# Kernel optimization log

Measured on AMD Instinct MI355X. Metric: run time of the kernel, lower is better.

The kernel has to match this reference:

```python
import jax, jax.numpy as jnp
import numpy as np
from jax import lax

B, T, H = 2, 1024, 2048
NH, D = 8, 128          # heads, head_dim
P = NH * D              # projection size
K = 4                   # short conv kernel size
EPS = 1e-6
SCALE = D ** -0.5


def _causal_conv_silu(x, w):
    # x: (B,T,C); w: (C,K) depthwise causal conv followed by silu (ShortConvolution)
    C = w.shape[0]
    kern = jnp.transpose(w)[:, None, :]  # (K,1,C)
    y = lax.conv_general_dilated(x, kern, window_strides=(1,), padding=[(K - 1, 0)],
                                 dimension_numbers=('NWC', 'WIO', 'NWC'),
                                 feature_group_count=C)
    return jax.nn.silu(y)


def _l2norm(x):
    return x * jax.lax.rsqrt(jnp.sum(x * x, axis=-1, keepdims=True) + EPS)


def _forward(hidden_states, Wq, Wk, Wv, conv_q, conv_k, conv_v, A_log, dt_bias,
             Wfa, Wfb, Wb, Wga, Wgb, norm_weight, Wo):
    x = hidden_states                                # (B,T,H)
    q = _causal_conv_silu(x @ Wq.T, conv_q)          # (B,T,P)
    k = _causal_conv_silu(x @ Wk.T, conv_k)
    v = _causal_conv_silu(x @ Wv.T, conv_v)
    # fused_kda_gate: g = -exp(A_log) * softplus(f_b(f_a(x)) + dt_bias), per (h,d) channel
    gf = (x @ Wfa.T) @ Wfb.T                         # (B,T,P) low-rank gate proj
    gf = gf.reshape(B, T, NH, D) + dt_bias.reshape(NH, D)
    g = -jnp.exp(A_log)[None, None, :, None] * jax.nn.softplus(gf)  # (B,T,NH,D) log-decay <= 0
    beta = jax.nn.sigmoid(x @ Wb.T)                  # (B,T,NH)
    q = _l2norm(q.reshape(B, T, NH, D)) * SCALE      # use_qk_l2norm_in_kernel + 1/sqrt(d) scale
    k = _l2norm(k.reshape(B, T, NH, D))
    v = v.reshape(B, T, NH, D)

    # gated delta-rule recurrence (KDA): per-key-channel decay, beta-weighted delta update
    def step(S, inp):
        q_t, k_t, v_t, g_t, b_t = inp                # (B,NH,D), beta (B,NH)
        S = S * jnp.exp(g_t)[..., None]              # decay rows (key dim) of S[.,.,dk,dv]
        kv = jnp.einsum('bhk,bhkv->bhv', k_t, S)
        delta = (v_t - kv) * b_t[..., None]
        S = S + jnp.einsum('bhk,bhv->bhkv', k_t, delta)
        o_t = jnp.einsum('bhk,bhkv->bhv', q_t, S)
        return S, o_t

    tfirst = lambda a: jnp.moveaxis(a, 1, 0)         # time-major for scan
    S0 = jnp.zeros((B, NH, D, D), x.dtype)
    _, o = lax.scan(step, S0, (tfirst(q), tfirst(k), tfirst(v), tfirst(g), tfirst(beta)))
    o = jnp.moveaxis(o, 0, 1)                        # (B,T,NH,D)

    # FusedRMSNormGated(sigmoid): gate applied before RMS normalization (Mamba2 convention)
    gate = ((x @ Wga.T) @ Wgb.T).reshape(B, T, NH, D)
    og = o * jax.nn.sigmoid(gate)
    og = og * jax.lax.rsqrt(jnp.mean(og * og, axis=-1, keepdims=True) + EPS) * norm_weight
    return og.reshape(B * T, P) @ Wo.T               # (B*T, H)


def setup_inputs():
    ks = jax.random.split(jax.random.key(0), 16)
    s = 0.02
    f32 = jnp.float32
    return {
        'hidden_states': jax.random.normal(ks[0], (B, T, H), f32),
        'Wq': jax.random.normal(ks[1], (P, H), f32) * s,
        'Wk': jax.random.normal(ks[2], (P, H), f32) * s,
        'Wv': jax.random.normal(ks[3], (P, H), f32) * s,
        'conv_q': jax.random.normal(ks[4], (P, K), f32) * 0.3,
        'conv_k': jax.random.normal(ks[5], (P, K), f32) * 0.3,
        'conv_v': jax.random.normal(ks[6], (P, K), f32) * 0.3,
        'A_log': jnp.log(jax.random.uniform(ks[7], (NH,), f32, 1.0, 16.0)),
        'dt_bias': jax.random.normal(ks[8], (P,), f32) * 0.5,
        'Wfa': jax.random.normal(ks[9], (D, H), f32) * s,
        'Wfb': jax.random.normal(ks[10], (P, D), f32) * s,
        'Wb': jax.random.normal(ks[11], (NH, H), f32) * s,
        'Wga': jax.random.normal(ks[12], (D, H), f32) * s,
        'Wgb': jax.random.normal(ks[13], (P, D), f32) * s,
        'norm_weight': jnp.ones((D,), f32),
        'Wo': jax.random.normal(ks[14], (H, P), f32) * s,
    }


def reference(hidden_states, Wq, Wk, Wv, conv_q, conv_k, conv_v, A_log, dt_bias,
              Wfa, Wfb, Wb, Wga, Wgb, norm_weight, Wo):
    return _forward(hidden_states, Wq, Wk, Wv, conv_q, conv_k, conv_v, A_log, dt_bias,
                    Wfa, Wfb, Wb, Wga, Wgb, norm_weight, Wo)
```

## Files before the change

### kernel.cpp

```cpp
#include <hip/hip_runtime.h>
#include <hip/hip_bf16.h>
#include <cstddef>
#include <cstdint>

#define Bb 2
#define Tt 1024
#define Hh 2048
#define NHh 8
#define Dd 128
#define Pp (NHh * Dd)
#define Kk 4
#define EPSf 1e-6f
#define SCALEf 0.08838834764831845f
#define DVQ 16
#define CHUNK 8

typedef short bf16x8 __attribute__((ext_vector_type(8)));
typedef float f32x4 __attribute__((ext_vector_type(4)));
typedef float f32x2 __attribute__((ext_vector_type(2)));

template <int CTRL>
__device__ __forceinline__ float dpp_add(float x) {
  int yi = __builtin_amdgcn_update_dpp(0, __builtin_bit_cast(int, x), CTRL, 0xF, 0xF, true);
  return x + __builtin_bit_cast(float, yi);
}
__device__ __forceinline__ float row16_sum(float x) {
  x = dpp_add<0xB1>(x);
  x = dpp_add<0x4E>(x);
  x = dpp_add<0x124>(x);
  x = dpp_add<0x128>(x);
  return x;
}

__device__ __forceinline__ void gload_lds16(const void* g, void* l) {
  __builtin_amdgcn_global_load_lds((const __attribute__((address_space(1))) void*)g,
                                   (__attribute__((address_space(3))) void*)l, 16, 0, 0);
}

__global__ __launch_bounds__(256) void cvt_bf16(const float* __restrict__ src,
                                                __hip_bfloat16* __restrict__ dst, int n) {
  const int i = (blockIdx.x * 256 + threadIdx.x) * 8;
  if (i >= n) return;
  const float4 a = *reinterpret_cast<const float4*>(src + i);
  const float4 b = *reinterpret_cast<const float4*>(src + i + 4);
  __hip_bfloat16 t[8];
  t[0] = __float2bfloat16(a.x); t[1] = __float2bfloat16(a.y);
  t[2] = __float2bfloat16(a.z); t[3] = __float2bfloat16(a.w);
  t[4] = __float2bfloat16(b.x); t[5] = __float2bfloat16(b.y);
  t[6] = __float2bfloat16(b.z); t[7] = __float2bfloat16(b.w);
  *reinterpret_cast<uint4*>(dst + i) = *reinterpret_cast<const uint4*>(t);
}

__global__ __launch_bounds__(256) void cvt_bf16_x4(const float* __restrict__ s0,
                                                   const float* __restrict__ s1,
                                                   const float* __restrict__ s2,
                                                   const float* __restrict__ s3,
                                                   __hip_bfloat16* __restrict__ d0,
                                                   __hip_bfloat16* __restrict__ d1,
                                                   __hip_bfloat16* __restrict__ d2,
                                                   __hip_bfloat16* __restrict__ d3,
                                                   int nper) {
  const int bpa = nper / 2048;
  const int a = blockIdx.x / bpa;
  const int i = (blockIdx.x % bpa) * 2048 + threadIdx.x * 8;
  const float* src = (a == 0) ? s0 : (a == 1) ? s1 : (a == 2) ? s2 : s3;
  __hip_bfloat16* dst = (a == 0) ? d0 : (a == 1) ? d1 : (a == 2) ? d2 : d3;
  const float4 x = *reinterpret_cast<const float4*>(src + i);
  const float4 y = *reinterpret_cast<const float4*>(src + i + 4);
  __hip_bfloat16 t[8];
  t[0] = __float2bfloat16(x.x); t[1] = __float2bfloat16(x.y);
  t[2] = __float2bfloat16(x.z); t[3] = __float2bfloat16(x.w);
  t[4] = __float2bfloat16(y.x); t[5] = __float2bfloat16(y.y);
  t[6] = __float2bfloat16(y.z); t[7] = __float2bfloat16(y.w);
  *reinterpret_cast<uint4*>(dst + i) = *reinterpret_cast<const uint4*>(t);
}

__global__ __launch_bounds__(256) void cvt_split(const float* __restrict__ src,
                                                 __hip_bfloat16* __restrict__ hi,
                                                 __hip_bfloat16* __restrict__ lo, int n) {
  const int i = (blockIdx.x * 256 + threadIdx.x) * 8;
  if (i >= n) return;
  __hip_bfloat16 th[8], tl[8];
#pragma unroll
  for (int j = 0; j < 2; j++) {
    const float4 a = *reinterpret_cast<const float4*>(src + i + j * 4);
    const float f[4] = {a.x, a.y, a.z, a.w};
#pragma unroll
    for (int e = 0; e < 4; e++) {
      const __hip_bfloat16 h = __float2bfloat16(f[e]);
      th[j * 4 + e] = h;
      tl[j * 4 + e] = __float2bfloat16(f[e] - __bfloat162float(h));
    }
  }
  *reinterpret_cast<uint4*>(hi + i) = *reinterpret_cast<const uint4*>(th);
  *reinterpret_cast<uint4*>(lo + i) = *reinterpret_cast<const uint4*>(tl);
}

__global__ __launch_bounds__(256) void transpose_f32(const float* __restrict__ src,
                                                     float* __restrict__ dst, int R, int C) {
  __shared__ float t[32][33];
  const int bx = blockIdx.x * 32, by = blockIdx.y * 32;
  const int tx = threadIdx.x & 31, ty = threadIdx.x >> 5;
#pragma unroll
  for (int i = ty; i < 32; i += 8) {
    const int r = by + i, c = bx + tx;
    if (r < R && c < C) t[i][tx] = src[(size_t)r * C + c];
  }
  __syncthreads();
#pragma unroll
  for (int i = ty; i < 32; i += 8) {
    const int c = bx + i, r = by + tx;
    if (c < C && r < R) dst[(size_t)c * R + r] = t[tx][i];
  }
}

__global__ __launch_bounds__(256) void gemm_bf16_lds(const __hip_bfloat16* __restrict__ A,
                                                     const __hip_bfloat16* __restrict__ B,
                                                     float* __restrict__ C,
                                                     __hip_bfloat16* __restrict__ Cbf,
                                                     int M, int N, int K, int outmode) {
  __shared__ __align__(16) __hip_bfloat16 As[128 * 64];
  __shared__ __align__(16) __hip_bfloat16 Bs[128 * 64];
  const int tid = threadIdx.x;
  const int wave = tid >> 6;
  const int lane = tid & 63;
  const int wm = (wave >> 1) * 64;
  const int wn = (wave & 1) * 64;
  const int bm = blockIdx.y * 128;
  const int bn = blockIdx.x * 128;
  const int l15 = lane & 15;
  const int l4 = lane >> 4;
  const int srow = lane >> 3;
  const int scol = (lane & 7) * 8;

  f32x4 acc[4][4];
#pragma unroll
  for (int i = 0; i < 4; i++)
#pragma unroll
    for (int j = 0; j < 4; j++) acc[i][j] = (f32x4){0.f, 0.f, 0.f, 0.f};

  for (int k0 = 0; k0 < K; k0 += 64) {
#pragma unroll
    for (int i = 0; i < 4; i++) {
      const int s = wave * 4 + i;
      const int row = s * 8 + srow;
      gload_lds16(A + (size_t)(bm + row) * K + k0 + scol, &As[s * 512]);
      gload_lds16(B + (size_t)(bn + row) * K + k0 + scol, &Bs[s * 512]);
    }
    __syncthreads();
    bf16x8 af[4][2], bfv[4][2];
#pragma unroll
    for (int kf = 0; kf < 2; kf++) {
      const int kc = kf * 32 + l4 * 8;
#pragma unroll
      for (int mf = 0; mf < 4; mf++)
        af[mf][kf] = *reinterpret_cast<const bf16x8*>(&As[(wm + mf * 16 + l15) * 64 + kc]);
#pragma unroll
      for (int nf = 0; nf < 4; nf++)
        bfv[nf][kf] = *reinterpret_cast<const bf16x8*>(&Bs[(wn + nf * 16 + l15) * 64 + kc]);
    }
#pragma unroll
    for (int kf = 0; kf < 2; kf++)
#pragma unroll
      for (int mf = 0; mf < 4; mf++)
#pragma unroll
        for (int nf = 0; nf < 4; nf++)
          acc[mf][nf] = __builtin_amdgcn_mfma_f32_16x16x32_bf16(af[mf][kf], bfv[nf][kf],
                                                                acc[mf][nf], 0, 0, 0);
    __syncthreads();
  }
#pragma unroll
  for (int mf = 0; mf < 4; mf++) {
#pragma unroll
    for (int nf = 0; nf < 4; nf++) {
      const int col = bn + wn + nf * 16 + l15;
#pragma unroll
      for (int r = 0; r < 4; r++) {
        const int row = bm + wm + mf * 16 + l4 * 4 + r;
        if (outmode == 0) C[(size_t)row * N + col] = acc[mf][nf][r];
        else Cbf[(size_t)row * N + col] = __float2bfloat16(acc[mf][nf][r]);
      }
    }
  }
}

__global__ __launch_bounds__(256) void gemm_bf16_3t_lds(const __hip_bfloat16* __restrict__ Ahi,
                                                        const __hip_bfloat16* __restrict__ Alo,
                                                        const __hip_bfloat16* __restrict__ Bhi,
                                                        const __hip_bfloat16* __restrict__ Blo,
                                                        float* __restrict__ C,
                                                        int M, int N, int K,
                                                        const float* __restrict__ dtb,
                                                        const float* __restrict__ A_log,
                                                        int gmode) {
  __shared__ __align__(16) __hip_bfloat16 Ahs[64 * 64];
  __shared__ __align__(16) __hip_bfloat16 Als[64 * 64];
  __shared__ __align__(16) __hip_bfloat16 Bhs[128 * 64];
  __shared__ __align__(16) __hip_bfloat16 Bls[128 * 64];
  const int tid = threadIdx.x;
  const int wave = tid >> 6;
  const int lane = tid & 63;
  const int wm = (wave >> 1) * 32;
  const int wn = (wave & 1) * 64;
  const int bm = blockIdx.y * 64;
  const int bn = blockIdx.x * 128;
  const int l15 = lane & 15;
  const int l4 = lane >> 4;
  const int srow = lane >> 3;
  const int scol = (lane & 7) * 8;

  f32x4 acc[2][4];
#pragma unroll
  for (int i = 0; i < 2; i++)
#pragma unroll
    for (int j = 0; j < 4; j++) acc[i][j] = (f32x4){0.f, 0.f, 0.f, 0.f};

  for (int k0 = 0; k0 < K; k0 += 64) {
#pragma unroll
    for (int i = 0; i < 12; i++) {
      const int sid = wave * 12 + i;
      if (sid < 8) {
        const int row = sid * 8 + srow;
        gload_lds16(Ahi + (size_t)(bm + row) * K + k0 + scol, &Ahs[sid * 512]);
      } else if (sid < 16) {
        const int row = (sid - 8) * 8 + srow;
        gload_lds16(Alo + (size_t)(bm + row) * K + k0 + scol, &Als[(sid - 8) * 512]);
      } else if (sid < 32) {
        const int row = (sid - 16) * 8 + srow;
        gload_lds16(Bhi + (size_t)(bn + row) * K + k0 + scol, &Bhs[(sid - 16) * 512]);
      } else {
        const int row = (sid - 32) * 8 + srow;
        gload_lds16(Blo + (size_t)(bn + row) * K + k0 + scol, &Bls[(sid - 32) * 512]);
      }
    }
    __syncthreads();
#pragma unroll
    for (int kf = 0; kf < 2; kf++) {
      const int kc = kf * 32 + l4 * 8;
      bf16x8 ah[2], al[2], bh[4], bl[4];
#pragma unroll
      for (int mf = 0; mf < 2; mf++) {
        ah[mf] = *reinterpret_cast<const bf16x8*>(&Ahs[(wm + mf * 16 + l15) * 64 + kc]);
        al[mf] = *reinterpret_cast<const bf16x8*>(&Als[(wm + mf * 16 + l15) * 64 + kc]);
      }
#pragma unroll
      for (int nf = 0; nf < 4; nf++) {
        bh[nf] = *reinterpret_cast<const bf16x8*>(&Bhs[(wn + nf * 16 + l15) * 64 + kc]);
        bl[nf] = *reinterpret_cast<const bf16x8*>(&Bls[(wn + nf * 16 + l15) * 64 + kc]);
      }
#pragma unroll
      for (int mf = 0; mf < 2; mf++)
#pragma unroll
        for (int nf = 0; nf < 4; nf++) {
          acc[mf][nf] = __builtin_amdgcn_mfma_f32_16x16x32_bf16(ah[mf], bh[nf], acc[mf][nf], 0, 0, 0);
          acc[mf][nf] = __builtin_amdgcn_mfma_f32_16x16x32_bf16(ah[mf], bl[nf], acc[mf][nf], 0, 0, 0);
          acc[mf][nf] = __builtin_amdgcn_mfma_f32_16x16x32_bf16(al[mf], bh[nf], acc[mf][nf], 0, 0, 0);
        }
    }
    __syncthreads();
  }
#pragma unroll
  for (int mf = 0; mf < 2; mf++)
#pragma unroll
    for (int nf = 0; nf < 4; nf++) {
      const int col = bn + wn + nf * 16 + l15;
#pragma unroll
      for (int r = 0; r < 4; r++) {
        const int row = bm + wm + mf * 16 + l4 * 4 + r;
        float val = acc[mf][nf][r];
        if (gmode) {
          const float xv = val + dtb[col];
          const float sp = (xv > 20.f) ? xv : log1pf(expf(xv));
          val = expf(-expf(A_log[col >> 7]) * sp);
        }
        C[(size_t)row * N + col] = val;
      }
    }
}

__global__ __launch_bounds__(256) void gemm_nt(const float* __restrict__ A,
                                               const float* __restrict__ Bm,
                                               float* __restrict__ C,
                                               int M, int N, int Kd) {
  __shared__ float As[16][64];
  __shared__ float Bs[16][64];
  const int bm = blockIdx.y * 64;
  const int bn = blockIdx.x * 64;
  const int tid = threadIdx.x;
  const int tx = tid & 15;
  const int ty = tid >> 4;
  const int lr = tid >> 2;
  const int lc = (tid & 3) << 2;
  float acc[4][4];
#pragma unroll
  for (int i = 0; i < 4; i++)
#pragma unroll
    for (int j = 0; j < 4; j++) acc[i][j] = 0.f;
  for (int k0 = 0; k0 < Kd; k0 += 16) {
    float4 a4 = make_float4(0.f, 0.f, 0.f, 0.f);
    float4 b4 = make_float4(0.f, 0.f, 0.f, 0.f);
    const int ar = bm + lr;
    if (ar < M) a4 = *reinterpret_cast<const float4*>(A + (size_t)ar * Kd + k0 + lc);
    const int br = bn + lr;
    if (br < N) b4 = *reinterpret_cast<const float4*>(Bm + (size_t)br * Kd + k0 + lc);
    As[lc + 0][lr] = a4.x; As[lc + 1][lr] = a4.y; As[lc + 2][lr] = a4.z; As[lc + 3][lr] = a4.w;
    Bs[lc + 0][lr] = b4.x; Bs[lc + 1][lr] = b4.y; Bs[lc + 2][lr] = b4.z; Bs[lc + 3][lr] = b4.w;
    __syncthreads();
#pragma unroll
    for (int kk = 0; kk < 16; kk++) {
      float4 av = *reinterpret_cast<const float4*>(&As[kk][ty << 2]);
      float4 bv = *reinterpret_cast<const float4*>(&Bs[kk][tx << 2]);
      float a[4] = {av.x, av.y, av.z, av.w};
      float b[4] = {bv.x, bv.y, bv.z, bv.w};
#pragma unroll
      for (int i = 0; i < 4; i++)
#pragma unroll
        for (int j = 0; j < 4; j++) acc[i][j] += a[i] * b[j];
    }
    __syncthreads();
  }
#pragma unroll
  for (int i = 0; i < 4; i++) {
    const int row = bm + (ty << 2) + i;
    if (row >= M) continue;
#pragma unroll
    for (int j = 0; j < 4; j++) {
      const int col = bn + (tx << 2) + j;
      if (col < N) C[(size_t)row * N + col] = acc[i][j];
    }
  }
}

__global__ __launch_bounds__(256) void beta_kernel(const float* __restrict__ x,
                                                   const float* __restrict__ Wb,
                                                   float* __restrict__ beta) {
  __shared__ float xs[Hh];
  const int m = blockIdx.x;
  const int tid = threadIdx.x;
  for (int i = tid; i < Hh; i += 256) xs[i] = x[(size_t)m * Hh + i];
  __syncthreads();
  const int h = tid >> 5;
  const int lane = tid & 31;
  float acc = 0.f;
  for (int i = lane; i < Hh; i += 32) acc += xs[i] * Wb[(size_t)h * Hh + i];
#pragma unroll
  for (int o = 16; o > 0; o >>= 1) acc += __shfl_down(acc, o, 32);
  if (lane == 0) beta[(size_t)m * NHh + h] = 1.f / (1.f + expf(-acc));
}

__global__ __launch_bounds__(256) void g_kernel(float* __restrict__ gbuf,
                                                const float* __restrict__ dtb,
                                                const float* __restrict__ A_log) {
  const size_t i = (size_t)blockIdx.x * 256 + threadIdx.x;
  const int c = (int)(i % Pp);
  const int h = c / Dd;
  const float xv = gbuf[i] + dtb[c];
  const float sp = (xv > 20.f) ? xv : log1pf(expf(xv));
  gbuf[i] = expf(-expf(A_log[h]) * sp);
}

__global__ __launch_bounds__(128) void conv_silu_norm(const float* __restrict__ xin,
                                                      const float* __restrict__ w,
                                                      float* __restrict__ out,
                                                      int mode, int instride, int coff) {
  const int idx = blockIdx.x;
  const int h = idx % NHh;
  const int bt = idx / NHh;
  const int t = bt % Tt;
  const int d = threadIdx.x;
  const int c = h * Dd + d;
  float acc = 0.f;
#pragma unroll
  for (int j = 0; j < Kk; j++) {
    const int tt = t - (Kk - 1) + j;
    float xv = 0.f;
    if (tt >= 0) xv = xin[(size_t)(bt - (Kk - 1) + j) * instride + coff + c];
    acc += w[c * Kk + j] * xv;
  }
  float y = acc / (1.f + expf(-acc));
  float r = y;
  if (mode > 0) {
    float ss = y * y;
#pragma unroll
    for (int o = 32; o > 0; o >>= 1) ss += __shfl_down(ss, o);
    __shared__ float red[2];
    if ((d & 63) == 0) red[d >> 6] = ss;
    __syncthreads();
    const float tot = red[0] + red[1];
    const float inv = rsqrtf(tot + EPSf);
    r = y * inv * (mode == 2 ? SCALEf : 1.f);
  }
  out[(size_t)bt * Pp + c] = r;
}

__global__ __launch_bounds__(128) void conv3_kernel(const float* __restrict__ qkvpre,
                                                    const float* __restrict__ cq,
                                                    const float* __restrict__ ck,
                                                    const float* __restrict__ cv,
                                                    float* __restrict__ outbase) {
  const int nblk = Bb * Tt * NHh;
  const int which = blockIdx.x / nblk;
  const int idx = blockIdx.x % nblk;
  const float* w = (which == 0) ? cq : (which == 1) ? ck : cv;
  const int mode = (which == 0) ? 2 : (which == 1) ? 1 : 0;
  const int h = idx % NHh;
  const int bt = idx / NHh;
  const int t = bt % Tt;
  const int d = threadIdx.x;
  const int c = h * Dd + d;
  float acc = 0.f;
#pragma unroll
  for (int j = 0; j < Kk; j++) {
    const int tt = t - (Kk - 1) + j;
    float xv = 0.f;
    if (tt >= 0) xv = qkvpre[(size_t)(bt - (Kk - 1) + j) * (4 * Pp) + which * Pp + c];
    acc += w[c * Kk + j] * xv;
  }
  float y = acc / (1.f + expf(-acc));
  float r = y;
  if (mode > 0) {
    float ss = y * y;
#pragma unroll
    for (int o = 32; o > 0; o >>= 1) ss += __shfl_down(ss, o);
    __shared__ float red[2];
    if ((d & 63) == 0) red[d >> 6] = ss;
    __syncthreads();
    const float tot = red[0] + red[1];
    const float inv = rsqrtf(tot + EPSf);
    r = y * inv * (mode == 2 ? SCALEf : 1.f);
  }
  outbase[(size_t)which * (Bb * Tt) * Pp + (size_t)bt * Pp + c] = r;
}

__global__ __launch_bounds__(128) void scan_kernel(const float* __restrict__ q,
                                                   const float* __restrict__ k,
                                                   const float* __restrict__ v,
                                                   const float* __restrict__ eg,
                                                   const float* __restrict__ beta,
                                                   float* __restrict__ o) {
  const int blk = blockIdx.x;
  const int bh = blk & 15;
  const int dvq = blk >> 4;
  const int b = bh >> 3, h = bh & 7;
  const int tid = threadIdx.x;
  const int qr = tid & 15;
  const int dvl = tid >> 4;
  const int dv = dvq * 8 + dvl;

  __shared__ __align__(16) float qs[2][CHUNK][16][12];
  __shared__ __align__(16) float ks[2][CHUNK][16][12];
  __shared__ __align__(16) float legs[2][CHUNK][16][12];
  __shared__ float vs[2][CHUNK][8];
  __shared__ float betas[2][CHUNK];

  f32x2 s2[4];
#pragma unroll
  for (int i = 0; i < 4; i++) s2[i] = (f32x2){0.f, 0.f};

  const size_t base = (size_t)(b * Tt) * Pp + h * Dd;
  const int le = tid;

  float rq[CHUNK], rk[CHUNK], re[CHUNK], rv[CHUNK], rb = 0.f;
  auto load_chunk = [&](int t0) {
    const size_t coff = base + (size_t)t0 * Pp;
#pragma unroll
    for (int j = 0; j < CHUNK; j++) {
      rq[j] = q[coff + (size_t)j * Pp + le];
      rk[j] = k[coff + (size_t)j * Pp + le];
      re[j] = eg[coff + (size_t)j * Pp + le];
    }
    if (tid < 8) {
#pragma unroll
      for (int j = 0; j < CHUNK; j++) rv[j] = v[coff + (size_t)j * Pp + dvq * 8 + tid];
    } else if (tid < 8 + CHUNK) {
      rb = beta[(size_t)(b * Tt + t0 + tid - 8) * NHh + h];
    }
  };
  auto write_lds = [&](int bufw) {
#pragma unroll
    for (int j = 0; j < CHUNK; j++) {
      qs[bufw][j][le >> 3][le & 7] = rq[j];
      ks[bufw][j][le >> 3][le & 7] = rk[j];
      legs[bufw][j][le >> 3][le & 7] = re[j];
    }
    if (tid < 8) {
#pragma unroll
      for (int j = 0; j < CHUNK; j++) vs[bufw][j][tid] = rv[j];
    } else if (tid < 8 + CHUNK) {
      betas[bufw][tid - 8] = rb;
    }
  };
  auto unpack = [](const float4& a, const float4& b, f32x2 out[4]) {
    out[0] = (f32x2){a.x, a.y}; out[1] = (f32x2){a.z, a.w};
    out[2] = (f32x2){b.x, b.y}; out[3] = (f32x2){b.z, b.w};
  };

  load_chunk(0);
  write_lds(0);
  __syncthreads();
  const int NC = Tt / CHUNK;
  size_t off = base;
  for (int c = 0; c < NC; c++) {
    if (c + 1 < NC) load_chunk((c + 1) * CHUNK);
    const int buf = c & 1;
    float vv[CHUNK], bb[CHUNK], opart[CHUNK];
#pragma unroll
    for (int j = 0; j < CHUNK; j++) { vv[j] = vs[buf][j][dvl]; bb[j] = betas[buf][j]; }

    f32x2 ck2[4], ce2[4], cq2[4], kt2[4];
    {
      const float4 k0 = *reinterpret_cast<const float4*>(&ks[buf][0][qr][0]);
      const float4 k1 = *reinterpret_cast<const float4*>(&ks[buf][0][qr][4]);
      const float4 e0 = *reinterpret_cast<const float4*>(&legs[buf][0][qr][0]);
      const float4 e1 = *reinterpret_cast<const float4*>(&legs[buf][0][qr][4]);
      const float4 q0 = *reinterpret_cast<const float4*>(&qs[buf][0][qr][0]);
      const float4 q1 = *reinterpret_cast<const float4*>(&qs[buf][0][qr][4]);
      unpack(k0, k1, ck2); unpack(e0, e1, ce2); unpack(q0, q1, cq2);
#pragma unroll
      for (int i = 0; i < 4; i++) kt2[i] = ck2[i] * ce2[i];
    }

#pragma unroll
    for (int j = 0; j < CHUNK; j++) {
      float4 nk0, nk1, ne0, ne1, nq0, nq1;
      if (j + 1 < CHUNK) {
        nk0 = *reinterpret_cast<const float4*>(&ks[buf][j + 1][qr][0]);
        nk1 = *reinterpret_cast<const float4*>(&ks[buf][j + 1][qr][4]);
        ne0 = *reinterpret_cast<const float4*>(&legs[buf][j + 1][qr][0]);
        ne1 = *reinterpret_cast<const float4*>(&legs[buf][j + 1][qr][4]);
        nq0 = *reinterpret_cast<const float4*>(&qs[buf][j + 1][qr][0]);
        nq1 = *reinterpret_cast<const float4*>(&qs[buf][j + 1][qr][4]);
      }
      f32x2 es0 = ce2[0] * s2[0], es1 = ce2[1] * s2[1];
      f32x2 es2v = ce2[2] * s2[2], es3 = ce2[3] * s2[3];
      f32x2 kva = kt2[0] * s2[0];
      f32x2 kvb = kt2[1] * s2[1];
      kva = kt2[2] * s2[2] + kva;
      kvb = kt2[3] * s2[3] + kvb;
      kva = kva + kvb;
      const float kvp = row16_sum(kva.x + kva.y);
      const float delta = (vv[j] - kvp) * bb[j];
      const f32x2 d2 = (f32x2){delta, delta};
      f32x2 o2;
      s2[0] = ck2[0] * d2 + es0;  o2 = cq2[0] * s2[0];
      s2[1] = ck2[1] * d2 + es1;  o2 = cq2[1] * s2[1] + o2;
      s2[2] = ck2[2] * d2 + es2v; o2 = cq2[2] * s2[2] + o2;
      s2[3] = ck2[3] * d2 + es3;  o2 = cq2[3] * s2[3] + o2;
      opart[j] = o2.x + o2.y;
      if (j + 1 < CHUNK) {
        unpack(nk0, nk1, ck2); unpack(ne0, ne1, ce2); unpack(nq0, nq1, cq2);
#pragma unroll
        for (int i = 0; i < 4; i++) kt2[i] = ck2[i] * ce2[i];
      }
    }
#pragma unroll
    for (int j = 0; j < CHUNK; j++) opart[j] = row16_sum(opart[j]);
    if (qr == 0) {
#pragma unroll
      for (int j = 0; j < CHUNK; j++) o[off + (size_t)j * Pp + dv] = opart[j];
    }
    if (c + 1 < NC) write_lds(buf ^ 1);
    __syncthreads();
    off += (size_t)CHUNK * Pp;
  }
}

__global__ __launch_bounds__(128) void gated_norm(float* __restrict__ o,
                                                  const float* __restrict__ gate,
                                                  int gstride,
                                                  const float* __restrict__ nw,
                                                  __hip_bfloat16* __restrict__ ogbf) {
  const int idx = blockIdx.x;
  const int h = idx % NHh;
  const int bt = idx / NHh;
  const int d = threadIdx.x;
  const size_t off = (size_t)bt * Pp + h * Dd;
  const float ov = o[off + d];
  const float gt = gate[(size_t)bt * gstride + h * Dd + d];
  const float val = ov / (1.f + expf(-gt));
  float ss = val * val;
#pragma unroll
  for (int sh = 32; sh > 0; sh >>= 1) ss += __shfl_down(ss, sh);
  __shared__ float red[2];
  if ((d & 63) == 0) red[d >> 6] = ss;
  __syncthreads();
  const float mean = (red[0] + red[1]) * (1.f / Dd);
  const float res = val * rsqrtf(mean + EPSf) * nw[d];
  if (ogbf != nullptr) ogbf[off + d] = __float2bfloat16(res);
  else o[off + d] = res;
}

extern "C" void kernel_launch(void* const* d_in, const int* in_sizes, int n_in,
                              void* d_out, int out_size, void* d_ws, size_t ws_size,
                              hipStream_t stream) {
  const float* x     = (const float*)d_in[0];
  const float* Wq    = (const float*)d_in[1];
  const float* Wk    = (const float*)d_in[2];
  const float* Wv    = (const float*)d_in[3];
  const float* cq    = (const float*)d_in[4];
  const float* ck    = (const float*)d_in[5];
  const float* cv    = (const float*)d_in[6];
  const float* A_log = (const float*)d_in[7];
  const float* dtb   = (const float*)d_in[8];
  const float* Wfa   = (const float*)d_in[9];
  const float* Wfb   = (const float*)d_in[10];
  const float* Wb    = (const float*)d_in[11];
  const float* Wga   = (const float*)d_in[12];
  const float* Wgb   = (const float*)d_in[13];
  const float* nw    = (const float*)d_in[14];
  const float* Wo    = (const float*)d_in[15];
  float* outp = (float*)d_out;

  const int M = Bb * Tt;
  const size_t MP = (size_t)M * Pp;
  float* ws = (float*)d_ws;
  float* qkvpre = ws;
  float* qb   = qkvpre + 4 * MP;
  float* kb   = qb + MP;
  float* vb   = kb + MP;
  float* gbuf = vb + MP;
  float* obuf = gbuf + MP;
  float* betab = obuf + MP;
  float* WfaT = betab + (size_t)M * NHh;
  float* WgaT = WfaT + (size_t)Hh * Dd;
  float* f32end = WgaT + (size_t)Hh * Dd;
  float* Wcombf = obuf;

  __hip_bfloat16* xhi    = (__hip_bfloat16*)f32end;
  __hip_bfloat16* xlo    = xhi + (size_t)M * Hh;
  __hip_bfloat16* Wqkvbf = xlo + (size_t)M * Hh;
  __hip_bfloat16* Wobf   = Wqkvbf + (size_t)4 * Pp * Hh;
  __hip_bfloat16* WfaThi = Wobf + (size_t)Hh * Pp;
  __hip_bfloat16* WfaTlo = WfaThi + (size_t)Hh * Dd;
  __hip_bfloat16* Wfbhi  = WfaTlo + (size_t)Hh * Dd;
  __hip_bfloat16* Wfblo  = Wfbhi + (size_t)Pp * Dd;
  __hip_bfloat16* WgaTbf = Wfblo + (size_t)Pp * Dd;
  __hip_bfloat16* Wgbbf  = WgaTbf + (size_t)Hh * Dd;
  __hip_bfloat16* Wcombhi = Wgbbf + (size_t)Pp * Dd;
  __hip_bfloat16* Wcomblo = Wcombhi + (size_t)Pp * Hh;
  __hip_bfloat16* end = Wcomblo + (size_t)Pp * Hh;
  __hip_bfloat16* ogbf = xlo;
  const bool use_mfma = ws_size >= (size_t)((char*)end - (char*)d_ws);

  const dim3 blk(256);
  if (use_mfma) {
    cvt_split<<<(int)((size_t)M * Hh / 2048), blk, 0, stream>>>(x, xhi, xlo, M * Hh);
    cvt_bf16_x4<<<4 * (int)((size_t)Pp * Hh / 2048), blk, 0, stream>>>(
        Wq, Wk, Wv, Wo, Wqkvbf, Wqkvbf + (size_t)Pp * Hh, Wqkvbf + (size_t)2 * Pp * Hh,
        Wobf, Pp * Hh);
    transpose_f32<<<dim3(Hh / 32, Dd / 32), blk, 0, stream>>>(Wfa, WfaT, Dd, Hh);
    transpose_f32<<<dim3(Hh / 32, Dd / 32), blk, 0, stream>>>(Wga, WgaT, Dd, Hh);
    cvt_split<<<(int)((size_t)Hh * Dd / 2048), blk, 0, stream>>>(WfaT, WfaThi, WfaTlo, Hh * Dd);
    cvt_split<<<(int)((size_t)Pp * Dd / 2048), blk, 0, stream>>>(Wfb, Wfbhi, Wfblo, Pp * Dd);
    cvt_bf16<<<(int)((size_t)Hh * Dd / 2048), blk, 0, stream>>>(WgaT, WgaTbf, Hh * Dd);
    cvt_bf16<<<(int)((size_t)Pp * Dd / 2048), blk, 0, stream>>>(Wgb, Wgbbf, Pp * Dd);
    gemm_bf16_3t_lds<<<dim3(Hh / 128, Pp / 64), blk, 0, stream>>>(Wfbhi, Wfblo, WfaThi, WfaTlo,
                                                                  Wcombf, Pp, Hh, Dd,
                                                                  nullptr, nullptr, 0);
    gemm_bf16_lds<<<dim3(Hh / 128, Pp / 128), blk, 0, stream>>>(Wgbbf, WgaTbf, nullptr,
                                                                Wqkvbf + (size_t)3 * Pp * Hh,
                                                                Pp, Hh, Dd, 1);
    cvt_split<<<(int)((size_t)Pp * Hh / 2048), blk, 0, stream>>>(Wcombf, Wcombhi, Wcomblo, Pp * Hh);
    gemm_bf16_lds<<<dim3(4 * Pp / 128, M / 128), blk, 0, stream>>>(xhi, Wqkvbf, qkvpre, nullptr,
                                                                   M, 4 * Pp, Hh, 0);
    gemm_bf16_3t_lds<<<dim3(Pp / 128, M / 64), blk, 0, stream>>>(xhi, xlo, Wcombhi, Wcomblo,
                                                                 gbuf, M, Pp, Hh,
                                                                 dtb, A_log, 1);
    beta_kernel<<<M, 256, 0, stream>>>(x, Wb, betab);
    conv3_kernel<<<3 * M * NHh, 128, 0, stream>>>(qkvpre, cq, ck, cv, qb);
    scan_kernel<<<Bb * NHh * DVQ, 128, 0, stream>>>(qb, kb, vb, gbuf, betab, obuf);
    gated_norm<<<M * NHh, 128, 0, stream>>>(obuf, qkvpre + (size_t)3 * Pp, 4 * Pp, nw, ogbf);
    gemm_bf16_lds<<<dim3(Hh / 128, M / 128), blk, 0, stream>>>(ogbf, Wobf, outp, nullptr, M, Hh, Pp, 0);
  } else {
    float* qpre = qkvpre;
    float* kpre = qkvpre + MP;
    float* vpre = qkvpre + 2 * MP;
    float* gate = qkvpre + 3 * MP;
    float* gfa = WfaT;
    float* gga = WgaT;
    gemm_nt<<<dim3(Pp / 64, M / 64), blk, 0, stream>>>(x, Wq, qpre, M, Pp, Hh);
    gemm_nt<<<dim3(Pp / 64, M / 64), blk, 0, stream>>>(x, Wk, kpre, M, Pp, Hh);
    gemm_nt<<<dim3(Pp / 64, M / 64), blk, 0, stream>>>(x, Wv, vpre, M, Pp, Hh);
    gemm_nt<<<dim3(Dd / 64, M / 64), blk, 0, stream>>>(x, Wfa, gfa, M, Dd, Hh);
    gemm_nt<<<dim3(Dd / 64, M / 64), blk, 0, stream>>>(x, Wga, gga, M, Dd, Hh);
    gemm_nt<<<dim3(Pp / 64, M / 64), blk, 0, stream>>>(gfa, Wfb, gbuf, M, Pp, Dd);
    gemm_nt<<<dim3(Pp / 64, M / 64), blk, 0, stream>>>(gga, Wgb, gate, M, Pp, Dd);
    beta_kernel<<<M, 256, 0, stream>>>(x, Wb, betab);
    g_kernel<<<(int)(MP / 256), 256, 0, stream>>>(gbuf, dtb, A_log);
    conv_silu_norm<<<M * NHh, 128, 0, stream>>>(qpre, cq, qb, 2, Pp, 0);
    conv_silu_norm<<<M * NHh, 128, 0, stream>>>(kpre, ck, kb, 1, Pp, 0);
    conv_silu_norm<<<M * NHh, 128, 0, stream>>>(vpre, cv, vb, 0, Pp, 0);
    scan_kernel<<<Bb * NHh * DVQ, 128, 0, stream>>>(qb, kb, vb, gbuf, betab, obuf);
    gated_norm<<<M * NHh, 128, 0, stream>>>(obuf, gate, Pp, nw, nullptr);
    gemm_nt<<<dim3(Hh / 64, M / 64), blk, 0, stream>>>(obuf, Wo, outp, M, Hh, Pp);
  }
}
```

Baseline: 456.7 us.

## Remap scan to one wave per value column with 64-lane key split

Rewrites the recurrent scan kernel so each wave owns one value column and its 64 lanes each hold two key rows of the state, instead of 16 lanes each holding eight. The grid doubles to 512 blocks of 256 threads, which raises parallelism and shortens each step's per-thread serial work. In exchange every step now needs a full 64-lane reduction through row-broadcast DPP plus a readlane, and the LDS layout becomes plain unpadded rows. More redundant loads of q, k and g are issued across the larger grid.

```diff
diff --git a/kernel.cpp b/kernel.cpp
--- a/kernel.cpp
+++ b/kernel.cpp
@@ -12,7 +12,7 @@
 #define Kk 4
 #define EPSf 1e-6f
 #define SCALEf 0.08838834764831845f
-#define DVQ 16
+#define DVQ32 32
 #define CHUNK 8
 
 typedef short bf16x8 __attribute__((ext_vector_type(8)));
@@ -29,6 +29,14 @@
   x = dpp_add<0x4E>(x);
   x = dpp_add<0x124>(x);
   x = dpp_add<0x128>(x);
+  return x;
+}
+__device__ __forceinline__ float wave64_sum_l63(float x) {
+  x = row16_sum(x);
+  int y1 = __builtin_amdgcn_update_dpp(0, __builtin_bit_cast(int, x), 0x142, 0xa, 0xF, false);
+  x = x + __builtin_bit_cast(float, y1);
+  int y2 = __builtin_amdgcn_update_dpp(0, __builtin_bit_cast(int, x), 0x143, 0xc, 0xF, false);
+  x = x + __builtin_bit_cast(float, y2);
   return x;
 }
 
@@ -432,7 +440,7 @@
   outbase[(size_t)which * (Bb * Tt) * Pp + (size_t)bt * Pp + c] = r;
 }
 
-__global__ __launch_bounds__(128) void scan_kernel(const float* __restrict__ q,
+__global__ __launch_bounds__(256) void scan_kernel(const float* __restrict__ q,
                                                    const float* __restrict__ k,
                                                    const float* __restrict__ v,
                                                    const float* __restrict__ eg,
@@ -443,56 +451,55 @@
   const int dvq = blk >> 4;
   const int b = bh >> 3, h = bh & 7;
   const int tid = threadIdx.x;
-  const int qr = tid & 15;
-  const int dvl = tid >> 4;
-  const int dv = dvq * 8 + dvl;
-
-  __shared__ __align__(16) float qs[2][CHUNK][16][12];
-  __shared__ __align__(16) float ks[2][CHUNK][16][12];
-  __shared__ __align__(16) float legs[2][CHUNK][16][12];
-  __shared__ float vs[2][CHUNK][8];
+  const int wave = tid >> 6;
+  const int lane = tid & 63;
+  const int dv = dvq * 4 + wave;
+
+  __shared__ __align__(16) float ks[2][CHUNK][Dd];
+  __shared__ __align__(16) float es[2][CHUNK][Dd];
+  __shared__ __align__(16) float qs[2][CHUNK][Dd];
+  __shared__ float vs[2][CHUNK][4];
   __shared__ float betas[2][CHUNK];
 
-  f32x2 s2[4];
-#pragma unroll
-  for (int i = 0; i < 4; i++) s2[i] = (f32x2){0.f, 0.f};
+  f32x2 s2 = (f32x2){0.f, 0.f};
 
   const size_t base = (size_t)(b * Tt) * Pp + h * Dd;
-  const int le = tid;
-
-  float rq[CHUNK], rk[CHUNK], re[CHUNK], rv[CHUNK], rb = 0.f;
+
+  float rk[4], re[4], rq[4], rv = 0.f, rb = 0.f;
   auto load_chunk = [&](int t0) {
     const size_t coff = base + (size_t)t0 * Pp;
 #pragma unroll
-    for (int j = 0; j < CHUNK; j++) {
-      rq[j] = q[coff + (size_t)j * Pp + le];
-      rk[j] = k[coff + (size_t)j * Pp + le];
-      re[j] = eg[coff + (size_t)j * Pp + le];
-    }
-    if (tid < 8) {
-#pragma unroll
-      for (int j = 0; j < CHUNK; j++) rv[j] = v[coff + (size_t)j * Pp + dvq * 8 + tid];
-    } else if (tid < 8 + CHUNK) {
-      rb = beta[(size_t)(b * Tt + t0 + tid - 8) * NHh + h];
+    for (int r = 0; r < 4; r++) {
+      const int idx = tid + r * 256;
+      const int c = idx >> 7, ch = idx & 127;
+      const size_t g = coff + (size_t)c * Pp + ch;
+      rk[r] = k[g];
+      re[r] = eg[g];
+      rq[r] = q[g];
+    }
+    if (tid < 32) {
+      const int c = tid >> 2, col = tid & 3;
+      rv = v[coff + (size_t)c * Pp + dvq * 4 + col];
+    } else if (tid < 32 + CHUNK) {
+      rb = beta[(size_t)(b * Tt + t0 + tid - 32) * NHh + h];
     }
   };
   auto write_lds = [&](int bufw) {
-#pragma unroll
-    for (int j = 0; j < CHUNK; j++) {
-      qs[bufw][j][le >> 3][le & 7] = rq[j];
-      ks[bufw][j][le >> 3][le & 7] = rk[j];
-      legs[bufw][j][le >> 3][le & 7] = re[j];
-    }
-    if (tid < 8) {
-#pragma unroll
-      for (int j = 0; j < CHUNK; j++) vs[bufw][j][tid] = rv[j];
-    } else if (tid < 8 + CHUNK) {
-      betas[bufw][tid - 8] = rb;
-    }
-  };
-  auto unpack = [](const float4& a, const float4& b, f32x2 out[4]) {
-    out[0] = (f32x2){a.x, a.y}; out[1] = (f32x2){a.z, a.w};
-    out[2] = (f32x2){b.x, b.y}; out[3] = (f32x2){b.z, b.w};
+    float* kf = &ks[bufw][0][0];
+    float* ef = &es[bufw][0][0];
+    float* qf = &qs[bufw][0][0];
+#pragma unroll
+    for (int r = 0; r < 4; r++) {
+      const int idx = tid + r * 256;
+      kf[idx] = rk[r];
+      ef[idx] = re[r];
+      qf[idx] = rq[r];
+    }
+    if (tid < 32) {
+      vs[bufw][tid >> 2][tid & 3] = rv;
+    } else if (tid < 32 + CHUNK) {
+      betas[bufw][tid - 32] = rb;
+    }
   };
 
   load_chunk(0);
@@ -505,57 +512,37 @@
     const int buf = c & 1;
     float vv[CHUNK], bb[CHUNK], opart[CHUNK];
 #pragma unroll
-    for (int j = 0; j < CHUNK; j++) { vv[j] = vs[buf][j][dvl]; bb[j] = betas[buf][j]; }
-
-    f32x2 ck2[4], ce2[4], cq2[4], kt2[4];
-    {
-      const float4 k0 = *reinterpret_cast<const float4*>(&ks[buf][0][qr][0]);
-      const float4 k1 = *reinterpret_cast<const float4*>(&ks[buf][0][qr][4]);
-      const float4 e0 = *reinterpret_cast<const float4*>(&legs[buf][0][qr][0]);
-      const float4 e1 = *reinterpret_cast<const float4*>(&legs[buf][0][qr][4]);
-      const float4 q0 = *reinterpret_cast<const float4*>(&qs[buf][0][qr][0]);
-      const float4 q1 = *reinterpret_cast<const float4*>(&qs[buf][0][qr][4]);
-      unpack(k0, k1, ck2); unpack(e0, e1, ce2); unpack(q0, q1, cq2);
-#pragma unroll
-      for (int i = 0; i < 4; i++) kt2[i] = ck2[i] * ce2[i];
-    }
+    for (int j = 0; j < CHUNK; j++) { vv[j] = vs[buf][j][wave]; bb[j] = betas[buf][j]; }
+
+    f32x2 ck = *reinterpret_cast<const f32x2*>(&ks[buf][0][lane * 2]);
+    f32x2 ce = *reinterpret_cast<const f32x2*>(&es[buf][0][lane * 2]);
+    f32x2 cq = *reinterpret_cast<const f32x2*>(&qs[buf][0][lane * 2]);
+    f32x2 kt = ck * ce;
 
 #pragma unroll
     for (int j = 0; j < CHUNK; j++) {
-      float4 nk0, nk1, ne0, ne1, nq0, nq1;
+      f32x2 nk, ne, nq;
       if (j + 1 < CHUNK) {
-        nk0 = *reinterpret_cast<const float4*>(&ks[buf][j + 1][qr][0]);
-        nk1 = *reinterpret_cast<const float4*>(&ks[buf][j + 1][qr][4]);
-        ne0 = *reinterpret_cast<const float4*>(&legs[buf][j + 1][qr][0]);
-        ne1 = *reinterpret_cast<const float4*>(&legs[buf][j + 1][qr][4]);
-        nq0 = *reinterpret_cast<const float4*>(&qs[buf][j + 1][qr][0]);
-        nq1 = *reinterpret_cast<const float4*>(&qs[buf][j + 1][qr][4]);
+        nk = *reinterpret_cast<const f32x2*>(&ks[buf][j + 1][lane * 2]);
+        ne = *reinterpret_cast<const f32x2*>(&es[buf][j + 1][lane * 2]);
+        nq = *reinterpret_cast<const f32x2*>(&qs[buf][j + 1][lane * 2]);
       }
-      f32x2 es0 = ce2[0] * s2[0], es1 = ce2[1] * s2[1];
-      f32x2 es2v = ce2[2] * s2[2], es3 = ce2[3] * s2[3];
-      f32x2 kva = kt2[0] * s2[0];
-      f32x2 kvb = kt2[1] * s2[1];
-      kva = kt2[2] * s2[2] + kva;
-      kvb = kt2[3] * s2[3] + kvb;
-      kva = kva + kvb;
-      const float kvp = row16_sum(kva.x + kva.y);
+      const f32x2 esv = ce * s2;
+      const f32x2 kv2 = kt * s2;
+      float kvl = kv2.x + kv2.y;
+      kvl = wave64_sum_l63(kvl);
+      const float kvp = __builtin_bit_cast(
+          float, __builtin_amdgcn_readlane(__builtin_bit_cast(int, kvl), 63));
       const float delta = (vv[j] - kvp) * bb[j];
       const f32x2 d2 = (f32x2){delta, delta};
-      f32x2 o2;
-      s2[0] = ck2[0] * d2 + es0;  o2 = cq2[0] * s2[0];
-      s2[1] = ck2[1] * d2 + es1;  o2 = cq2[1] * s2[1] + o2;
-      s2[2] = ck2[2] * d2 + es2v; o2 = cq2[2] * s2[2] + o2;
-      s2[3] = ck2[3] * d2 + es3;  o2 = cq2[3] * s2[3] + o2;
+      s2 = ck * d2 + esv;
+      const f32x2 o2 = cq * s2;
       opart[j] = o2.x + o2.y;
-      if (j + 1 < CHUNK) {
-        unpack(nk0, nk1, ck2); unpack(ne0, ne1, ce2); unpack(nq0, nq1, cq2);
-#pragma unroll
-        for (int i = 0; i < 4; i++) kt2[i] = ck2[i] * ce2[i];
-      }
-    }
-#pragma unroll
-    for (int j = 0; j < CHUNK; j++) opart[j] = row16_sum(opart[j]);
-    if (qr == 0) {
+      if (j + 1 < CHUNK) { ck = nk; ce = ne; cq = nq; kt = ck * ce; }
+    }
+#pragma unroll
+    for (int j = 0; j < CHUNK; j++) opart[j] = wave64_sum_l63(opart[j]);
+    if (lane == 63) {
 #pragma unroll
       for (int j = 0; j < CHUNK; j++) o[off + (size_t)j * Pp + dv] = opart[j];
     }
@@ -668,7 +655,7 @@
                                                                  dtb, A_log, 1);
     beta_kernel<<<M, 256, 0, stream>>>(x, Wb, betab);
     conv3_kernel<<<3 * M * NHh, 128, 0, stream>>>(qkvpre, cq, ck, cv, qb);
-    scan_kernel<<<Bb * NHh * DVQ, 128, 0, stream>>>(qb, kb, vb, gbuf, betab, obuf);
+    scan_kernel<<<Bb * NHh * DVQ32, 256, 0, stream>>>(qb, kb, vb, gbuf, betab, obuf);
     gated_norm<<<M * NHh, 128, 0, stream>>>(obuf, qkvpre + (size_t)3 * Pp, 4 * Pp, nw, ogbf);
     gemm_bf16_lds<<<dim3(Hh / 128, M / 128), blk, 0, stream>>>(ogbf, Wobf, outp, nullptr, M, Hh, Pp, 0);
   } else {
@@ -690,7 +677,7 @@
     conv_silu_norm<<<M * NHh, 128, 0, stream>>>(qpre, cq, qb, 2, Pp, 0);
     conv_silu_norm<<<M * NHh, 128, 0, stream>>>(kpre, ck, kb, 1, Pp, 0);
     conv_silu_norm<<<M * NHh, 128, 0, stream>>>(vpre, cv, vb, 0, Pp, 0);
-    scan_kernel<<<Bb * NHh * DVQ, 128, 0, stream>>>(qb, kb, vb, gbuf, betab, obuf);
+    scan_kernel<<<Bb * NHh * DVQ32, 256, 0, stream>>>(qb, kb, vb, gbuf, betab, obuf);
     gated_norm<<<M * NHh, 128, 0, stream>>>(obuf, gate, Pp, nw, nullptr);
     gemm_nt<<<dim3(Hh / 64, M / 64), blk, 0, stream>>>(obuf, Wo, outp, M, Hh, Pp);
   }
```

After: 486.9 us. 6.6% more time.

## Fold beta projection into QKV GEMM and compute low-rank weight products with fp32 SIMT GEMM

Applied to the files above, without the earlier changes.

Precomputing the combined low-rank gate weights (Wfb·Wfa, Wgb·Wga) now uses a direct fp32 NN GEMM that writes bf16 hi/lo output. This replaces the earlier chain of transposes, bf16 splits and MFMA GEMMs plus a final split pass. The beta projection Wb is appended as extra rows (NW=4224) to the fused QKV+gate weight matrix, which removes beta_kernel, and the scan applies the sigmoid on load. The aim is fewer launches and less conversion traffic. The trade-off is that beta is now computed from a bf16 x and bf16 Wb rather than in fp32.

```diff
diff --git a/kernel.cpp b/kernel.cpp
--- a/kernel.cpp
+++ b/kernel.cpp
@@ -9,6 +9,7 @@
 #define NHh 8
 #define Dd 128
 #define Pp (NHh * Dd)
+#define NW 4224
 #define Kk 4
 #define EPSf 1e-6f
 #define SCALEf 0.08838834764831845f
@@ -96,21 +97,60 @@
   *reinterpret_cast<uint4*>(lo + i) = *reinterpret_cast<const uint4*>(tl);
 }
 
-__global__ __launch_bounds__(256) void transpose_f32(const float* __restrict__ src,
-                                                     float* __restrict__ dst, int R, int C) {
-  __shared__ float t[32][33];
-  const int bx = blockIdx.x * 32, by = blockIdx.y * 32;
-  const int tx = threadIdx.x & 31, ty = threadIdx.x >> 5;
-#pragma unroll
-  for (int i = ty; i < 32; i += 8) {
-    const int r = by + i, c = bx + tx;
-    if (r < R && c < C) t[i][tx] = src[(size_t)r * C + c];
-  }
-  __syncthreads();
-#pragma unroll
-  for (int i = ty; i < 32; i += 8) {
-    const int c = bx + i, r = by + tx;
-    if (c < C && r < R) dst[(size_t)c * R + r] = t[tx][i];
+__global__ __launch_bounds__(256) void gemm_nn_split(const float* __restrict__ A,
+                                                     const float* __restrict__ B,
+                                                     __hip_bfloat16* __restrict__ Chi,
+                                                     __hip_bfloat16* __restrict__ Clo,
+                                                     int M, int N, int K, int mode) {
+  __shared__ float As[64][33];
+  __shared__ float Bs[32][65];
+  const int bm = blockIdx.y * 64, bn = blockIdx.x * 64;
+  const int tid = threadIdx.x;
+  const int tx = tid & 15, ty = tid >> 4;
+  float acc[4][4];
+#pragma unroll
+  for (int i = 0; i < 4; i++)
+#pragma unroll
+    for (int j = 0; j < 4; j++) acc[i][j] = 0.f;
+  for (int k0 = 0; k0 < K; k0 += 32) {
+#pragma unroll
+    for (int i = 0; i < 8; i++) {
+      const int idx = tid + i * 256;
+      const int r = idx >> 5, c = idx & 31;
+      As[r][c] = A[(size_t)(bm + r) * K + k0 + c];
+    }
+#pragma unroll
+    for (int i = 0; i < 8; i++) {
+      const int idx = tid + i * 256;
+      const int r = idx >> 6, c = idx & 63;
+      Bs[r][c] = B[(size_t)(k0 + r) * N + bn + c];
+    }
+    __syncthreads();
+#pragma unroll
+    for (int kk = 0; kk < 32; kk++) {
+      float a[4], b[4];
+#pragma unroll
+      for (int i = 0; i < 4; i++) a[i] = As[ty * 4 + i][kk];
+#pragma unroll
+      for (int j = 0; j < 4; j++) b[j] = Bs[kk][tx * 4 + j];
+#pragma unroll
+      for (int i = 0; i < 4; i++)
+#pragma unroll
+        for (int j = 0; j < 4; j++) acc[i][j] += a[i] * b[j];
+    }
+    __syncthreads();
+  }
+#pragma unroll
+  for (int i = 0; i < 4; i++) {
+    const int row = bm + ty * 4 + i;
+#pragma unroll
+    for (int j = 0; j < 4; j++) {
+      const int col = bn + tx * 4 + j;
+      const float v = acc[i][j];
+      const __hip_bfloat16 h = __float2bfloat16(v);
+      Chi[(size_t)row * N + col] = h;
+      if (mode == 0) Clo[(size_t)row * N + col] = __float2bfloat16(v - __bfloat162float(h));
+    }
   }
 }
 
@@ -397,7 +437,8 @@
                                                     const float* __restrict__ cq,
                                                     const float* __restrict__ ck,
                                                     const float* __restrict__ cv,
-                                                    float* __restrict__ outbase) {
+                                                    float* __restrict__ outbase,
+                                                    int instride) {
   const int nblk = Bb * Tt * NHh;
   const int which = blockIdx.x / nblk;
   const int idx = blockIdx.x % nblk;
@@ -413,7 +454,7 @@
   for (int j = 0; j < Kk; j++) {
     const int tt = t - (Kk - 1) + j;
     float xv = 0.f;
-    if (tt >= 0) xv = qkvpre[(size_t)(bt - (Kk - 1) + j) * (4 * Pp) + which * Pp + c];
+    if (tt >= 0) xv = qkvpre[(size_t)(bt - (Kk - 1) + j) * instride + which * Pp + c];
     acc += w[c * Kk + j] * xv;
   }
   float y = acc / (1.f + expf(-acc));
@@ -436,7 +477,8 @@
                                                    const float* __restrict__ k,
                                                    const float* __restrict__ v,
                                                    const float* __restrict__ eg,
-                                                   const float* __restrict__ beta,
+                                                   const float* __restrict__ betasrc,
+                                                   int bstride, int bcol, int bsig,
                                                    float* __restrict__ o) {
   const int blk = blockIdx.x;
   const int bh = blk & 15;
@@ -473,7 +515,8 @@
 #pragma unroll
       for (int j = 0; j < CHUNK; j++) rv[j] = v[coff + (size_t)j * Pp + dvq * 8 + tid];
     } else if (tid < 8 + CHUNK) {
-      rb = beta[(size_t)(b * Tt + t0 + tid - 8) * NHh + h];
+      const float brw = betasrc[(size_t)(b * Tt + t0 + tid - 8) * bstride + bcol + h];
+      rb = bsig ? 1.f / (1.f + expf(-brw)) : brw;
     }
   };
   auto write_lds = [&](int bufw) {
@@ -615,28 +658,21 @@
   const size_t MP = (size_t)M * Pp;
   float* ws = (float*)d_ws;
   float* qkvpre = ws;
-  float* qb   = qkvpre + 4 * MP;
+  float* qb   = qkvpre + (size_t)M * NW;
   float* kb   = qb + MP;
   float* vb   = kb + MP;
   float* gbuf = vb + MP;
   float* obuf = gbuf + MP;
   float* betab = obuf + MP;
-  float* WfaT = betab + (size_t)M * NHh;
-  float* WgaT = WfaT + (size_t)Hh * Dd;
-  float* f32end = WgaT + (size_t)Hh * Dd;
-  float* Wcombf = obuf;
+  float* gfa  = betab + (size_t)M * NHh;
+  float* gga  = gfa + (size_t)M * Dd;
+  float* f32end = gga + (size_t)M * Dd;
 
   __hip_bfloat16* xhi    = (__hip_bfloat16*)f32end;
   __hip_bfloat16* xlo    = xhi + (size_t)M * Hh;
   __hip_bfloat16* Wqkvbf = xlo + (size_t)M * Hh;
-  __hip_bfloat16* Wobf   = Wqkvbf + (size_t)4 * Pp * Hh;
-  __hip_bfloat16* WfaThi = Wobf + (size_t)Hh * Pp;
-  __hip_bfloat16* WfaTlo = WfaThi + (size_t)Hh * Dd;
-  __hip_bfloat16* Wfbhi  = WfaTlo + (size_t)Hh * Dd;
-  __hip_bfloat16* Wfblo  = Wfbhi + (size_t)Pp * Dd;
-  __hip_bfloat16* WgaTbf = Wfblo + (size_t)Pp * Dd;
-  __hip_bfloat16* Wgbbf  = WgaTbf + (size_t)Hh * Dd;
-  __hip_bfloat16* Wcombhi = Wgbbf + (size_t)Pp * Dd;
+  __hip_bfloat16* Wobf   = Wqkvbf + (size_t)NW * Hh;
+  __hip_bfloat16* Wcombhi = Wobf + (size_t)Hh * Pp;
   __hip_bfloat16* Wcomblo = Wcombhi + (size_t)Pp * Hh;
   __hip_bfloat16* end = Wcomblo + (size_t)Pp * Hh;
   __hip_bfloat16* ogbf = xlo;
@@ -648,36 +684,28 @@
     cvt_bf16_x4<<<4 * (int)((size_t)Pp * Hh / 2048), blk, 0, stream>>>(
         Wq, Wk, Wv, Wo, Wqkvbf, Wqkvbf + (size_t)Pp * Hh, Wqkvbf + (size_t)2 * Pp * Hh,
         Wobf, Pp * Hh);
-    transpose_f32<<<dim3(Hh / 32, Dd / 32), blk, 0, stream>>>(Wfa, WfaT, Dd, Hh);
-    transpose_f32<<<dim3(Hh / 32, Dd / 32), blk, 0, stream>>>(Wga, WgaT, Dd, Hh);
-    cvt_split<<<(int)((size_t)Hh * Dd / 2048), blk, 0, stream>>>(WfaT, WfaThi, WfaTlo, Hh * Dd);
-    cvt_split<<<(int)((size_t)Pp * Dd / 2048), blk, 0, stream>>>(Wfb, Wfbhi, Wfblo, Pp * Dd);
-    cvt_bf16<<<(int)((size_t)Hh * Dd / 2048), blk, 0, stream>>>(WgaT, WgaTbf, Hh * Dd);
-    cvt_bf16<<<(int)((size_t)Pp * Dd / 2048), blk, 0, stream>>>(Wgb, Wgbbf, Pp * Dd);
-    gemm_bf16_3t_lds<<<dim3(Hh / 128, Pp / 64), blk, 0, stream>>>(Wfbhi, Wfblo, WfaThi, WfaTlo,
-                                                                  Wcombf, Pp, Hh, Dd,
-                                                                  nullptr, nullptr, 0);
-    gemm_bf16_lds<<<dim3(Hh / 128, Pp / 128), blk, 0, stream>>>(Wgbbf, WgaTbf, nullptr,
-                                                                Wqkvbf + (size_t)3 * Pp * Hh,
-                                                                Pp, Hh, Dd, 1);
-    cvt_split<<<(int)((size_t)Pp * Hh / 2048), blk, 0, stream>>>(Wcombf, Wcombhi, Wcomblo, Pp * Hh);
-    gemm_bf16_lds<<<dim3(4 * Pp / 128, M / 128), blk, 0, stream>>>(xhi, Wqkvbf, qkvpre, nullptr,
-                                                                   M, 4 * Pp, Hh, 0);
+    cvt_bf16<<<(NHh * Hh) / 2048, blk, 0, stream>>>(Wb, Wqkvbf + (size_t)4096 * Hh, NHh * Hh);
+    gemm_nn_split<<<dim3(Hh / 64, Pp / 64), blk, 0, stream>>>(Wfb, Wfa, Wcombhi, Wcomblo,
+                                                              Pp, Hh, Dd, 0);
+    gemm_nn_split<<<dim3(Hh / 64, Pp / 64), blk, 0, stream>>>(Wgb, Wga,
+                                                              Wqkvbf + (size_t)3 * Pp * Hh,
+                                                              nullptr, Pp, Hh, Dd, 1);
+    gemm_bf16_lds<<<dim3(NW / 128, M / 128), blk, 0, stream>>>(xhi, Wqkvbf, qkvpre, nullptr,
+                                                               M, NW, Hh, 0);
     gemm_bf16_3t_lds<<<dim3(Pp / 128, M / 64), blk, 0, stream>>>(xhi, xlo, Wcombhi, Wcomblo,
                                                                  gbuf, M, Pp, Hh,
                                                                  dtb, A_log, 1);
-    beta_kernel<<<M, 256, 0, stream>>>(x, Wb, betab);
-    conv3_kernel<<<3 * M * NHh, 128, 0, stream>>>(qkvpre, cq, ck, cv, qb);
-    scan_kernel<<<Bb * NHh * DVQ, 128, 0, stream>>>(qb, kb, vb, gbuf, betab, obuf);
-    gated_norm<<<M * NHh, 128, 0, stream>>>(obuf, qkvpre + (size_t)3 * Pp, 4 * Pp, nw, ogbf);
-    gemm_bf16_lds<<<dim3(Hh / 128, M / 128), blk, 0, stream>>>(ogbf, Wobf, outp, nullptr, M, Hh, Pp, 0);
+    conv3_kernel<<<3 * M * NHh, 128, 0, stream>>>(qkvpre, cq, ck, cv, qb, NW);
+    scan_kernel<<<Bb * NHh * DVQ, 128, 0, stream>>>(qb, kb, vb, gbuf,
+                                                    qkvpre, NW, 4096, 1, obuf);
+    gated_norm<<<M * NHh, 128, 0, stream>>>(obuf, qkvpre + (size_t)3 * Pp, NW, nw, ogbf);
+    gemm_bf16_lds<<<dim3(Hh / 128, M / 128), blk, 0, stream>>>(ogbf, Wobf, outp, nullptr,
+                                                               M, Hh, Pp, 0);
   } else {
     float* qpre = qkvpre;
     float* kpre = qkvpre + MP;
     float* vpre = qkvpre + 2 * MP;
     float* gate = qkvpre + 3 * MP;
-    float* gfa = WfaT;
-    float* gga = WgaT;
     gemm_nt<<<dim3(Pp / 64, M / 64), blk, 0, stream>>>(x, Wq, qpre, M, Pp, Hh);
     gemm_nt<<<dim3(Pp / 64, M / 64), blk, 0, stream>>>(x, Wk, kpre, M, Pp, Hh);
     gemm_nt<<<dim3(Pp / 64, M / 64), blk, 0, stream>>>(x, Wv, vpre, M, Pp, Hh);
@@ -690,7 +718,8 @@
     conv_silu_norm<<<M * NHh, 128, 0, stream>>>(qpre, cq, qb, 2, Pp, 0);
     conv_silu_norm<<<M * NHh, 128, 0, stream>>>(kpre, ck, kb, 1, Pp, 0);
     conv_silu_norm<<<M * NHh, 128, 0, stream>>>(vpre, cv, vb, 0, Pp, 0);
-    scan_kernel<<<Bb * NHh * DVQ, 128, 0, stream>>>(qb, kb, vb, gbuf, betab, obuf);
+    scan_kernel<<<Bb * NHh * DVQ, 128, 0, stream>>>(qb, kb, vb, gbuf,
+                                                    betab, NHh, 0, 0, obuf);
     gated_norm<<<M * NHh, 128, 0, stream>>>(obuf, gate, Pp, nw, nullptr);
     gemm_nt<<<dim3(Hh / 64, M / 64), blk, 0, stream>>>(obuf, Wo, outp, M, Hh, Pp);
   }
```

Result: slower. 503.7 us (+10.3%).
